# Kernel tuning notes

Measured on AMD Instinct MI355X. Metric: run time of the kernel, lower is better.

## Reference

```python
import jax, jax.numpy as jnp
import numpy as np

DIM = 768
HEADS = 12
HEAD_DIM = DIM // HEADS  # 64
B, T = 4, 2048


def setup_inputs() -> dict:
    key = jax.random.key(0)
    k1, k2, k3 = jax.random.split(key, 3)
    x = jax.random.normal(k1, (B, T, DIM), dtype=jnp.float32)
    w_qkv = jax.random.normal(k2, (DIM, 3 * DIM), dtype=jnp.float32) * (DIM ** -0.5)
    w_out = jax.random.normal(k3, (DIM, DIM), dtype=jnp.float32) * (DIM ** -0.5)
    b_out = jnp.zeros((DIM,), dtype=jnp.float32)
    return {"x": x, "w_qkv": w_qkv, "w_out": w_out, "b_out": b_out}


def reference(x, w_qkv, w_out, b_out):
    b, t, _ = x.shape
    # fused QKV projection (no bias)
    xp = x @ w_qkv                               # (b, t, 3*dim)
    # faithful to einops 'b t (d k h) -> k b h t d' with k=3, h=HEADS
    xp = xp.reshape(b, t, HEAD_DIM, 3, HEADS)
    qkv = jnp.transpose(xp, (3, 0, 4, 1, 2))     # (3, b, h, t, d)
    q, k, v = qkv[0], qkv[1], qkv[2]
    scores = jnp.einsum('bhid,bhjd->bhij', q, k) * (HEAD_DIM ** -0.5)
    attn = jax.nn.softmax(scores, axis=-1)
    out = jnp.einsum('bhij,bhjd->bhid', attn, v)  # (b, h, t, d)
    out = jnp.transpose(out, (0, 2, 1, 3)).reshape(b, t, HEADS * HEAD_DIM)
    return out @ w_out + b_out
```

## Files before the change

### kernel.cpp

```cpp
#include <hip/hip_runtime.h>
#include <hip/hip_bf16.h>


typedef short short8 __attribute__((ext_vector_type(8)));
typedef _Float16 half8 __attribute__((ext_vector_type(8)));
typedef float f32x16 __attribute__((ext_vector_type(16)));
typedef unsigned int uint4v __attribute__((ext_vector_type(4)));
typedef unsigned short ushort8v __attribute__((ext_vector_type(8)));
typedef unsigned short ushort4v __attribute__((ext_vector_type(4)));
typedef unsigned short ushort;

__device__ __forceinline__ ushort f2h(float x) {
    _Float16 h = (_Float16)x;
    return __builtin_bit_cast(ushort, h);
}
__device__ __forceinline__ unsigned pk2h(float lo, float hi) {
    return __builtin_bit_cast(unsigned, __builtin_amdgcn_cvt_pkrtz(lo, hi));
}
__device__ __forceinline__ short8 ldfrag(const ushort* buf, int row, int slotLogical) {
    int phys = slotLogical ^ (row & 7);
    return *reinterpret_cast<const short8*>(&buf[row * 64 + phys * 8]);
}
__device__ __forceinline__ f32x16 mfma16(half8 a, half8 b, f32x16 c) {
    return __builtin_amdgcn_mfma_f32_32x32x16_f16(a, b, c, 0, 0, 0);
}
__device__ __forceinline__ half8 ldfragh(const ushort* buf, int row, int slotLogical) {
    return __builtin_bit_cast(half8, ldfrag(buf, row, slotLogical));
}
__device__ __forceinline__ void gload16(const ushort* g, ushort* l) {
    __builtin_amdgcn_global_load_lds((__attribute__((address_space(1))) void*)g,
                                     (__attribute__((address_space(3))) void*)l, 16, 0, 0);
}

__global__ __launch_bounds__(256) void cast_x(const float* __restrict__ x,
                                              ushort* __restrict__ Xh) {
    long i8 = (long)(blockIdx.x * 256 + threadIdx.x) * 8;
    float4 v0 = *reinterpret_cast<const float4*>(&x[i8]);
    float4 v1 = *reinterpret_cast<const float4*>(&x[i8 + 4]);
    float v[8] = {v0.x, v0.y, v0.z, v0.w, v1.x, v1.y, v1.z, v1.w};
    ushort8v hh;
#pragma unroll
    for (int j = 0; j < 8; ++j) hh[j] = f2h(v[j]);
    *reinterpret_cast<ushort8v*>(&Xh[i8]) = hh;
}

__global__ __launch_bounds__(256) void prep_wqkv(const float* __restrict__ w,
                                                 ushort* __restrict__ Wt) {
    int id = blockIdx.x * 256 + threadIdx.x;
    int n = id % 2304;
    int oct = id / 2304;
    int g = n >> 6, d = n & 63;
    int col = d * 36 + g;
    ushort8v hh;
#pragma unroll
    for (int i = 0; i < 8; ++i) hh[i] = f2h(w[(long)(8 * oct + i) * 2304 + col]);
    *reinterpret_cast<ushort8v*>(&Wt[(long)n * 768 + 8 * oct]) = hh;
}

__global__ __launch_bounds__(256) void prep_wout(const float* __restrict__ w,
                                                 ushort* __restrict__ Wo) {
    int id = blockIdx.x * 256 + threadIdx.x;
    int n = id % 768;
    int oct = id / 768;
    ushort8v hh;
#pragma unroll
    for (int i = 0; i < 8; ++i) hh[i] = f2h(w[(long)(8 * oct + i) * 768 + n]);
    *reinterpret_cast<ushort8v*>(&Wo[(long)n * 768 + 8 * oct]) = hh;
}

__device__ __forceinline__ void gemm_core(const ushort* __restrict__ A,
                                          const ushort* __restrict__ Bt,
                                          long aBase, long bBase,
                                          ushort* sA, ushort* sB, f32x16 (&acc)[2][2]) {
    const int tid = threadIdx.x;
    const int lane = tid & 63, w = tid >> 6;
    const int c31 = lane & 31, g1 = lane >> 5;
    const int wr = w >> 1, wc = w & 1;
    const int srow_in_chunk = lane >> 3;
    for (int k0 = 0; k0 < 768; k0 += 64) {
        __syncthreads();
#pragma unroll
        for (int t = 0; t < 4; ++t) {
            int row = w * 32 + t * 8 + srow_in_chunk;
            int sl = (lane & 7) ^ (row & 7);
            long goff = (long)row * 768 + k0 + sl * 8;
            int ldst = (w * 32 + t * 8) * 64;
            gload16(&A[aBase + goff], &sA[ldst]);
            gload16(&Bt[bBase + goff], &sB[ldst]);
        }
        __syncthreads();
#pragma unroll
        for (int ks = 0; ks < 4; ++ks) {
            half8 ah[2], bh[2];
#pragma unroll
            for (int i = 0; i < 2; ++i) {
                ah[i] = ldfragh(sA, wr * 64 + i * 32 + c31, 2 * ks + g1);
                bh[i] = ldfragh(sB, wc * 64 + i * 32 + c31, 2 * ks + g1);
            }
#pragma unroll
            for (int mi = 0; mi < 2; ++mi)
#pragma unroll
                for (int nj = 0; nj < 2; ++nj)
                    acc[mi][nj] = mfma16(ah[mi], bh[nj], acc[mi][nj]);
        }
    }
}

__global__ __launch_bounds__(256) void gemm_qkv(const ushort* __restrict__ Xh,
                                                const ushort* __restrict__ Wt,
                                                ushort* __restrict__ Qf,
                                                ushort* __restrict__ Kf,
                                                ushort* __restrict__ Vt) {
    __shared__ ushort sA[128 * 64];
    __shared__ ushort sB[128 * 64];
    const int by0 = blockIdx.y * 128, bx0 = blockIdx.x * 128;
    f32x16 acc[2][2] = {};
    gemm_core(Xh, Wt, (long)by0 * 768, (long)bx0 * 768, sA, sB, acc);

    const int tid = threadIdx.x, lane = tid & 63, w = tid >> 6;
    const int c31 = lane & 31, g1 = lane >> 5;
    const int wr = w >> 1, wc = w & 1;
    const int bb = by0 >> 11, tb = by0 & 2047;
#pragma unroll
    for (int nj = 0; nj < 2; ++nj) {
        int n = bx0 + wc * 64 + nj * 32 + c31;
        int gg = n >> 6;
        int d = n & 63;
        if (gg < 24) {
            int kq = gg >= 12;
            int hh = gg - kq * 12;
            ushort* Dst = kq ? Kf : Qf;
            float sc = kq ? 0.1803368801111204f : 1.0f;
            long cb = ((long)(bb * 12 + hh) * 2048) * 64 + d;
#pragma unroll
            for (int mi = 0; mi < 2; ++mi)
#pragma unroll
                for (int r = 0; r < 16; ++r) {
                    int t = tb + wr * 64 + mi * 32 + (r & 3) + 8 * (r >> 2) + 4 * g1;
                    Dst[cb + (long)t * 64] = f2h(acc[mi][nj][r] * sc);
                }
        } else {
            int hh = gg - 24;
            long vb = ((long)(bb * 12 + hh) * 64 + d) * 2048;
#pragma unroll
            for (int mi = 0; mi < 2; ++mi)
#pragma unroll
                for (int rq = 0; rq < 4; ++rq) {
                    int tq = tb + wr * 64 + mi * 32 + 8 * rq + 4 * g1;
                    ushort4v vv;
#pragma unroll
                    for (int j = 0; j < 4; ++j) vv[j] = f2h(acc[mi][nj][4 * rq + j]);
                    *reinterpret_cast<ushort4v*>(&Vt[vb + tq]) = vv;
                }
        }
    }
}

__global__ __launch_bounds__(256) void flash_attn(const ushort* __restrict__ Qf,
                                                  const ushort* __restrict__ Kf,
                                                  const ushort* __restrict__ Vt,
                                                  ushort* __restrict__ Of) {
    __shared__ ushort Ks[3][64 * 64];
    __shared__ ushort Vs[3][64 * 64];
    const int tid = threadIdx.x;
    const int w = tid >> 6;
    const int lane = tid & 63;
    const int c = lane & 31, g1 = lane >> 5;
    const int wgid = blockIdx.x;
    const int xblk = (wgid >> 3) & 15;
    const int bh = (wgid & 7) + 8 * (wgid >> 7);
    const int t0 = xblk * 128 + w * 32;
    const long hb = (long)bh * 2048 * 64;

    half8 qh[4];
    {
        const long qrow = hb + (long)(t0 + c) * 64;
#pragma unroll
        for (int ks = 0; ks < 4; ++ks)
            qh[ks] = __builtin_bit_cast(half8, *reinterpret_cast<const short8*>(&Qf[qrow + ks * 16 + g1 * 8]));
    }

    const int r0 = tid >> 3, sl = tid & 7, r1 = r0 + 32;
    const int off0 = r0 * 64 + ((sl ^ (r0 & 7)) * 8);
    const int off1 = r1 * 64 + ((sl ^ (r1 & 7)) * 8);

    {
        short8 k00 = *reinterpret_cast<const short8*>(&Kf[hb + (long)r0 * 64 + sl * 8]);
        short8 k01 = *reinterpret_cast<const short8*>(&Kf[hb + (long)r1 * 64 + sl * 8]);
        short8 v00 = *reinterpret_cast<const short8*>(&Vt[hb + (long)r0 * 2048 + sl * 8]);
        short8 v01 = *reinterpret_cast<const short8*>(&Vt[hb + (long)r1 * 2048 + sl * 8]);
        short8 k10 = *reinterpret_cast<const short8*>(&Kf[hb + (long)(64 + r0) * 64 + sl * 8]);
        short8 k11 = *reinterpret_cast<const short8*>(&Kf[hb + (long)(64 + r1) * 64 + sl * 8]);
        short8 v10 = *reinterpret_cast<const short8*>(&Vt[hb + (long)r0 * 2048 + 64 + sl * 8]);
        short8 v11 = *reinterpret_cast<const short8*>(&Vt[hb + (long)r1 * 2048 + 64 + sl * 8]);
        *reinterpret_cast<short8*>(&Ks[0][off0]) = k00;
        *reinterpret_cast<short8*>(&Ks[0][off1]) = k01;
        *reinterpret_cast<short8*>(&Vs[0][off0]) = v00;
        *reinterpret_cast<short8*>(&Vs[0][off1]) = v01;
        *reinterpret_cast<short8*>(&Ks[1][off0]) = k10;
        *reinterpret_cast<short8*>(&Ks[1][off1]) = k11;
        *reinterpret_cast<short8*>(&Vs[1][off0]) = v10;
        *reinterpret_cast<short8*>(&Vs[1][off1]) = v11;
    }
    __syncthreads();

    f32x16 s0 = {}, s1 = {};
#pragma unroll
    for (int ks = 0; ks < 4; ++ks) {
        int slot = 2 * ks + g1;
        half8 k0f = ldfragh(&Ks[0][0], c, slot);
        half8 k1f = ldfragh(&Ks[0][0], 32 + c, slot);
        s0 = mfma16(k0f, qh[ks], s0);
        s1 = mfma16(k1f, qh[ks], s1);
    }

    f32x16 o0 = {}, o1 = {};
    float lrun = 0.f;
    int p = 0;

    for (int j = 0; j < 32; ++j) {
        const bool hasN1 = j + 1 < 32;
        const bool hasN2 = j + 2 < 32;
        const int p1 = (p + 1 == 3) ? 0 : p + 1;
        const int p2 = (p + 2 >= 3) ? p + 2 - 3 : p + 2;

        f32x16 n0 = {}, n1 = {};
        if (hasN1) {
            __builtin_amdgcn_s_setprio(1);
#pragma unroll
            for (int ks = 0; ks < 4; ++ks) {
                int slot = 2 * ks + g1;
                half8 k0f = ldfragh(&Ks[p1][0], c, slot);
                half8 k1f = ldfragh(&Ks[p1][0], 32 + c, slot);
                n0 = mfma16(k0f, qh[ks], n0);
                n1 = mfma16(k1f, qh[ks], n1);
            }
            __builtin_amdgcn_s_setprio(0);
        }

        short8 pk0, pk1, pv0, pv1;
        if (hasN2) {
            int jn = (j + 2) * 64;
            pk0 = *reinterpret_cast<const short8*>(&Kf[hb + (long)(jn + r0) * 64 + sl * 8]);
            pk1 = *reinterpret_cast<const short8*>(&Kf[hb + (long)(jn + r1) * 64 + sl * 8]);
            pv0 = *reinterpret_cast<const short8*>(&Vt[hb + (long)r0 * 2048 + jn + sl * 8]);
            pv1 = *reinterpret_cast<const short8*>(&Vt[hb + (long)r1 * 2048 + jn + sl * 8]);
        }

#pragma unroll
        for (int r = 0; r < 16; ++r) {
            s0[r] = exp2f(s0[r]);
            s1[r] = exp2f(s1[r]);
            lrun += s0[r] + s1[r];
        }

        __builtin_amdgcn_s_setprio(1);
#pragma unroll
        for (int ks = 0; ks < 4; ++ks) {
            const int b8 = (ks & 1) * 8;
            uint4v dv;
#pragma unroll
            for (int mi = 0; mi < 2; ++mi) {
                float aLo = (ks < 2) ? s0[2 * mi + b8] : s1[2 * mi + b8];
                float aHi = (ks < 2) ? s0[2 * mi + b8 + 1] : s1[2 * mi + b8 + 1];
                float bLo = (ks < 2) ? s0[2 * mi + b8 + 4] : s1[2 * mi + b8 + 4];
                float bHi = (ks < 2) ? s0[2 * mi + b8 + 5] : s1[2 * mi + b8 + 5];
                unsigned xA = pk2h(aLo, aHi);
                unsigned xB = pk2h(bLo, bHi);
                auto rr = __builtin_amdgcn_permlane32_swap(xA, xB, false, false);
                dv[mi] = rr[0];
                dv[2 + mi] = rr[1];
            }
            half8 pb = __builtin_bit_cast(half8, dv);
            int slot = 2 * ks + g1;
            half8 va0 = ldfragh(&Vs[p][0], c, slot);
            half8 va1 = ldfragh(&Vs[p][0], 32 + c, slot);
            o0 = mfma16(va0, pb, o0);
            o1 = mfma16(va1, pb, o1);
        }
        __builtin_amdgcn_s_setprio(0);

        if (hasN2) {
            *reinterpret_cast<short8*>(&Ks[p2][off0]) = pk0;
            *reinterpret_cast<short8*>(&Ks[p2][off1]) = pk1;
            *reinterpret_cast<short8*>(&Vs[p2][off0]) = pv0;
            *reinterpret_cast<short8*>(&Vs[p2][off1]) = pv1;
        }
        __syncthreads();

        s0 = n0; s1 = n1;
        p = p1;
    }

    const float ltot = lrun + __shfl_xor(lrun, 32);
    const float inv = 1.0f / ltot;
    const int bb = bh / 12, h = bh - bb * 12;
    const long obase = ((long)(bb * 2048 + t0 + c)) * 768 + h * 64;
#pragma unroll
    for (int m = 0; m < 4; ++m) {
        int d0 = 8 * m + 4 * g1;
        ushort4v a, b;
#pragma unroll
        for (int j = 0; j < 4; ++j) {
            a[j] = f2h(o0[4 * m + j] * inv);
            b[j] = f2h(o1[4 * m + j] * inv);
        }
        *reinterpret_cast<ushort4v*>(&Of[obase + d0]) = a;
        *reinterpret_cast<ushort4v*>(&Of[obase + 32 + d0]) = b;
    }
}

__global__ __launch_bounds__(256) void gemm_out(const ushort* __restrict__ Of,
                                                const ushort* __restrict__ Wo,
                                                const float* __restrict__ bias,
                                                float* __restrict__ Cout) {
    __shared__ ushort sA[128 * 64];
    __shared__ ushort sB[128 * 64];
    const int by0 = blockIdx.y * 128, bx0 = blockIdx.x * 128;
    f32x16 acc[2][2] = {};
    gemm_core(Of, Wo, (long)by0 * 768, (long)bx0 * 768, sA, sB, acc);

    const int tid = threadIdx.x, lane = tid & 63, w = tid >> 6;
    const int c31 = lane & 31, g1 = lane >> 5;
    const int wr = w >> 1, wc = w & 1;
#pragma unroll
    for (int nj = 0; nj < 2; ++nj) {
        int n = bx0 + wc * 64 + nj * 32 + c31;
        float bv = bias[n];
#pragma unroll
        for (int mi = 0; mi < 2; ++mi)
#pragma unroll
            for (int r = 0; r < 16; ++r) {
                int row = by0 + wr * 64 + mi * 32 + (r & 3) + 8 * (r >> 2) + 4 * g1;
                Cout[(long)row * 768 + n] = acc[mi][nj][r] + bv;
            }
    }
}

extern "C" void kernel_launch(void* const* d_in, const int* in_sizes, int n_in,
                              void* d_out, int out_size, void* d_ws, size_t ws_size,
                              hipStream_t stream) {
    const float* x     = (const float*)d_in[0];
    const float* w_qkv = (const float*)d_in[1];
    const float* w_out = (const float*)d_in[2];
    const float* b_out = (const float*)d_in[3];
    float* out = (float*)d_out;

    const long U = 12582912;
    char* p = (char*)d_ws;
    ushort* Xh = (ushort*)(p);
    ushort* Wt = (ushort*)(p + U);
    ushort* Wo = (ushort*)(p + U + 3538944);
    ushort* Qf = (ushort*)(p + U + 4718592);
    ushort* Kf = Qf + 6291456;
    ushort* Vt = Kf + 6291456;
    ushort* Of = Xh;

    cast_x    <<<3072, 256, 0, stream>>>(x, Xh);
    prep_wqkv <<<864, 256, 0, stream>>>(w_qkv, Wt);
    prep_wout <<<288, 256, 0, stream>>>(w_out, Wo);
    gemm_qkv  <<<dim3(18, 64), 256, 0, stream>>>(Xh, Wt, Qf, Kf, Vt);
    flash_attn<<<768, 256, 0, stream>>>(Qf, Kf, Vt, Of);
    gemm_out  <<<dim3(6, 64), 256, 0, stream>>>(Of, Wo, b_out, out);
}
```

Baseline: 186.6 us.

## Merge prep kernels, compute softmax row sums via MFMA, use pointer increments

Merges the three cast/transpose prep kernels into one launch, which removes two kernel launches and their gaps. In flash attention, the softmax denominator now comes from an extra MFMA of a ones vector against the packed P fragments, replacing the scalar adds and the final cross-lane shuffle. The K/V prefetch addresses become running pointers instead of being recomputed each iteration. The extra MFMA adds matrix work per step, and the denominator now sums the fp16-rounded probabilities instead of the fp32 values.

```diff
diff --git a/kernel.cpp b/kernel.cpp
--- a/kernel.cpp
+++ b/kernel.cpp
@@ -32,40 +32,41 @@
                                      (__attribute__((address_space(3))) void*)l, 16, 0, 0);
 }
 
-__global__ __launch_bounds__(256) void cast_x(const float* __restrict__ x,
-                                              ushort* __restrict__ Xh) {
-    long i8 = (long)(blockIdx.x * 256 + threadIdx.x) * 8;
-    float4 v0 = *reinterpret_cast<const float4*>(&x[i8]);
-    float4 v1 = *reinterpret_cast<const float4*>(&x[i8 + 4]);
-    float v[8] = {v0.x, v0.y, v0.z, v0.w, v1.x, v1.y, v1.z, v1.w};
-    ushort8v hh;
-#pragma unroll
-    for (int j = 0; j < 8; ++j) hh[j] = f2h(v[j]);
-    *reinterpret_cast<ushort8v*>(&Xh[i8]) = hh;
-}
-
-__global__ __launch_bounds__(256) void prep_wqkv(const float* __restrict__ w,
-                                                 ushort* __restrict__ Wt) {
-    int id = blockIdx.x * 256 + threadIdx.x;
-    int n = id % 2304;
-    int oct = id / 2304;
-    int g = n >> 6, d = n & 63;
-    int col = d * 36 + g;
-    ushort8v hh;
-#pragma unroll
-    for (int i = 0; i < 8; ++i) hh[i] = f2h(w[(long)(8 * oct + i) * 2304 + col]);
-    *reinterpret_cast<ushort8v*>(&Wt[(long)n * 768 + 8 * oct]) = hh;
-}
-
-__global__ __launch_bounds__(256) void prep_wout(const float* __restrict__ w,
-                                                 ushort* __restrict__ Wo) {
-    int id = blockIdx.x * 256 + threadIdx.x;
-    int n = id % 768;
-    int oct = id / 768;
-    ushort8v hh;
-#pragma unroll
-    for (int i = 0; i < 8; ++i) hh[i] = f2h(w[(long)(8 * oct + i) * 768 + n]);
-    *reinterpret_cast<ushort8v*>(&Wo[(long)n * 768 + 8 * oct]) = hh;
+__global__ __launch_bounds__(256) void prep_all(const float* __restrict__ x,
+                                                const float* __restrict__ wqkv,
+                                                const float* __restrict__ wout,
+                                                ushort* __restrict__ Xh,
+                                                ushort* __restrict__ Wt,
+                                                ushort* __restrict__ Wo) {
+    int b = blockIdx.x;
+    if (b < 3072) {
+        long i8 = (long)(b * 256 + threadIdx.x) * 8;
+        float4 v0 = *reinterpret_cast<const float4*>(&x[i8]);
+        float4 v1 = *reinterpret_cast<const float4*>(&x[i8 + 4]);
+        float v[8] = {v0.x, v0.y, v0.z, v0.w, v1.x, v1.y, v1.z, v1.w};
+        ushort8v hh;
+#pragma unroll
+        for (int j = 0; j < 8; ++j) hh[j] = f2h(v[j]);
+        *reinterpret_cast<ushort8v*>(&Xh[i8]) = hh;
+    } else if (b < 3072 + 864) {
+        int id = (b - 3072) * 256 + threadIdx.x;
+        int n = id % 2304;
+        int oct = id / 2304;
+        int g = n >> 6, d = n & 63;
+        int col = d * 36 + g;
+        ushort8v hh;
+#pragma unroll
+        for (int i = 0; i < 8; ++i) hh[i] = f2h(wqkv[(long)(8 * oct + i) * 2304 + col]);
+        *reinterpret_cast<ushort8v*>(&Wt[(long)n * 768 + 8 * oct]) = hh;
+    } else {
+        int id = (b - 3936) * 256 + threadIdx.x;
+        int n = id % 768;
+        int oct = id / 768;
+        ushort8v hh;
+#pragma unroll
+        for (int i = 0; i < 8; ++i) hh[i] = f2h(wout[(long)(8 * oct + i) * 768 + n]);
+        *reinterpret_cast<ushort8v*>(&Wo[(long)n * 768 + 8 * oct]) = hh;
+    }
 }
 
 __device__ __forceinline__ void gemm_core(const ushort* __restrict__ A,
@@ -204,6 +205,11 @@
     }
     __syncthreads();
 
+    const ushort* kst0 = &Kf[hb + (long)(128 + r0) * 64 + sl * 8];
+    const ushort* kst1 = &Kf[hb + (long)(128 + r1) * 64 + sl * 8];
+    const ushort* vst0 = &Vt[hb + (long)r0 * 2048 + 128 + sl * 8];
+    const ushort* vst1 = &Vt[hb + (long)r1 * 2048 + 128 + sl * 8];
+
     f32x16 s0 = {}, s1 = {};
 #pragma unroll
     for (int ks = 0; ks < 4; ++ks) {
@@ -214,8 +220,11 @@
         s1 = mfma16(k1f, qh[ks], s1);
     }
 
-    f32x16 o0 = {}, o1 = {};
-    float lrun = 0.f;
+    half8 onesv;
+#pragma unroll
+    for (int i = 0; i < 8; ++i) onesv[i] = (_Float16)1.0f;
+
+    f32x16 o0 = {}, o1 = {}, olacc = {};
     int p = 0;
 
     for (int j = 0; j < 32; ++j) {
@@ -240,18 +249,18 @@
 
         short8 pk0, pk1, pv0, pv1;
         if (hasN2) {
-            int jn = (j + 2) * 64;
-            pk0 = *reinterpret_cast<const short8*>(&Kf[hb + (long)(jn + r0) * 64 + sl * 8]);
-            pk1 = *reinterpret_cast<const short8*>(&Kf[hb + (long)(jn + r1) * 64 + sl * 8]);
-            pv0 = *reinterpret_cast<const short8*>(&Vt[hb + (long)r0 * 2048 + jn + sl * 8]);
-            pv1 = *reinterpret_cast<const short8*>(&Vt[hb + (long)r1 * 2048 + jn + sl * 8]);
+            pk0 = *reinterpret_cast<const short8*>(kst0);
+            pk1 = *reinterpret_cast<const short8*>(kst1);
+            pv0 = *reinterpret_cast<const short8*>(vst0);
+            pv1 = *reinterpret_cast<const short8*>(vst1);
+            kst0 += 4096; kst1 += 4096;
+            vst0 += 64;   vst1 += 64;
         }
 
 #pragma unroll
         for (int r = 0; r < 16; ++r) {
             s0[r] = exp2f(s0[r]);
             s1[r] = exp2f(s1[r]);
-            lrun += s0[r] + s1[r];
         }
 
         __builtin_amdgcn_s_setprio(1);
@@ -277,6 +286,7 @@
             half8 va1 = ldfragh(&Vs[p][0], 32 + c, slot);
             o0 = mfma16(va0, pb, o0);
             o1 = mfma16(va1, pb, o1);
+            olacc = mfma16(onesv, pb, olacc);
         }
         __builtin_amdgcn_s_setprio(0);
 
@@ -292,8 +302,7 @@
         p = p1;
     }
 
-    const float ltot = lrun + __shfl_xor(lrun, 32);
-    const float inv = 1.0f / ltot;
+    const float inv = 1.0f / olacc[0];
     const int bb = bh / 12, h = bh - bb * 12;
     const long obase = ((long)(bb * 2048 + t0 + c)) * 768 + h * 64;
 #pragma unroll
@@ -356,9 +365,7 @@
     ushort* Vt = Kf + 6291456;
     ushort* Of = Xh;
 
-    cast_x    <<<3072, 256, 0, stream>>>(x, Xh);
-    prep_wqkv <<<864, 256, 0, stream>>>(w_qkv, Wt);
-    prep_wout <<<288, 256, 0, stream>>>(w_out, Wo);
+    prep_all  <<<4224, 256, 0, stream>>>(x, w_qkv, w_out, Xh, Wt, Wo);
     gemm_qkv  <<<dim3(18, 64), 256, 0, stream>>>(Xh, Wt, Qf, Kf, Vt);
     flash_attn<<<768, 256, 0, stream>>>(Qf, Kf, Vt, Of);
     gemm_out  <<<dim3(6, 64), 256, 0, stream>>>(Of, Wo, b_out, out);
```

New measurement: 189.9 us. About the same (+1.7%).
